# Kernel tuning notes

Hardware: AMD Instinct MI355X
Metric: run time of the kernel (lower is better)

Reference implementation:

```python
import jax, jax.numpy as jnp
import numpy as np

OUT = 3      # pooled output size (fmap_size//4 = 14//4 = 3)
RATIO = 2    # roi_align sampling ratio (fixed; torchvision adaptive ratio for 14/3 bins is 2)
P = 20       # num_persons


def _bilinear(fm, y, x):
    # fm: [C,H,W]; y,x broadcastable coordinate grids. torchvision aligned=False semantics.
    C, H, W = fm.shape
    y, x = jnp.broadcast_arrays(y, x)
    valid = (y > -1.0) & (y < H) & (x > -1.0) & (x < W)
    y = jnp.clip(y, 0.0, H - 1.0)
    x = jnp.clip(x, 0.0, W - 1.0)
    y0 = jnp.floor(y).astype(jnp.int32)
    x0 = jnp.floor(x).astype(jnp.int32)
    y1 = jnp.minimum(y0 + 1, H - 1)
    x1 = jnp.minimum(x0 + 1, W - 1)
    ly = y - y0
    lx = x - x0
    hy = 1.0 - ly
    hx = 1.0 - lx
    v00 = fm[:, y0, x0]
    v01 = fm[:, y0, x1]
    v10 = fm[:, y1, x0]
    v11 = fm[:, y1, x1]
    val = hy * hx * v00 + hy * lx * v01 + ly * hx * v10 + ly * lx * v11
    return jnp.where(valid, val, 0.0)  # [C, ...]


def _roi_align_one(fm, box):
    # fm: [C,H,W], box: [4] = (x1,y1,x2,y2) in feature-map coords -> [C,OUT,OUT]
    x1, y1, x2, y2 = box
    bw = (x2 - x1) / OUT
    bh = (y2 - y1) / OUT
    off = (jnp.arange(OUT * RATIO, dtype=fm.dtype) + 0.5) / RATIO  # bin-unit offsets
    xs = x1 + off * bw
    ys = y1 + off * bh
    vals = _bilinear(fm, ys[:, None], xs[None, :])  # [C, OUT*RATIO, OUT*RATIO]
    C = fm.shape[0]
    return vals.reshape(C, OUT, RATIO, OUT, RATIO).mean(axis=(2, 4))


def setup_inputs() -> dict:
    key = jax.random.key(0)
    ks = jax.random.split(key, 8)
    B, N, NB, C, FS = 128, 8, 27, 1024, 14
    fmap = jax.random.normal(ks[0], (B, C, FS, FS), jnp.float32)
    # boxes in feature-map coordinates with x1<x2, y1<y2
    lo = jax.random.uniform(ks[1], (B, N, 2), jnp.float32) * 10.0
    ext = 2.0 + jax.random.uniform(ks[2], (B, N, 2), jnp.float32) * 4.0
    hi = jnp.minimum(lo + ext, float(FS))
    boxes = jnp.concatenate([lo, hi], axis=-1)  # [B,N,4] (x1,y1,x2,y2)
    # unique person ids per frame (scatter target indices)
    pids = jax.vmap(lambda k: jax.random.permutation(k, P)[:N])(jax.random.split(ks[3], B)).astype(jnp.int32)
    w1 = jax.random.normal(ks[4], (512, C), jnp.float32) * 0.02
    w2 = jax.random.normal(ks[5], (256, 512), jnp.float32) * 0.05
    fc1_w = jax.random.normal(ks[6], (1024, 256 * OUT * OUT), jnp.float32) * 0.02
    fc1_b = jnp.zeros((1024,), jnp.float32)
    fc2_w = jax.random.normal(ks[7], (27, 1024), jnp.float32) * 0.02
    fc2_b = jnp.zeros((27,), jnp.float32)
    return {"fmap": fmap, "boxes": boxes, "pids": pids, "w1": w1, "w2": w2,
            "fc1_w": fc1_w, "fc1_b": fc1_b, "fc2_w": fc2_w, "fc2_b": fc2_b}


def _forward(fmap, boxes, pids, w1, w2, fc1_w, fc1_b, fc2_w, fc2_b):
    B, N = boxes.shape[:2]
    # per-image, per-box ROI align: [B,N,C,3,3]
    roi = jax.vmap(jax.vmap(_roi_align_one, in_axes=(None, 0)), in_axes=(0, 0))(fmap, boxes)
    # behavior_conv: two bias-free 1x1 convs (no nonlinearity between)
    h = jnp.einsum('bnchw,oc->bnohw', roi, w1)
    h = jnp.einsum('bnchw,oc->bnohw', h, w2)  # [B,N,256,3,3]
    feat = h.reshape(B, N, -1)                # [B,N,2304]
    bidx = jnp.broadcast_to(jnp.arange(B)[:, None], (B, N))
    # scatter into behavior_tensor keyed by person id (unique pids per frame -> well-defined)
    bt = jnp.zeros((B, P, feat.shape[-1]), feat.dtype).at[bidx, pids].set(feat)
    mean_b = bt.mean(axis=0)                  # [P,2304] mean over batch
    cur = bt[bidx, pids]                      # [B,N,2304]
    diff = mean_b[pids] - cur
    # behavior_fc (dropout is identity at inference)
    h1 = jax.nn.relu(jnp.einsum('bnd,hd->bnh', diff, fc1_w) + fc1_b)
    return jnp.einsum('bnh,oh->bno', h1, fc2_w) + fc2_b  # [B,N,num_behaviors]


def reference(fmap, boxes, pids, w1, w2, fc1_w, fc1_b, fc2_w, fc2_b):
    # fmap is detached and roi_align runs under no_grad in the original
    return _forward(jax.lax.stop_gradient(fmap), jax.lax.stop_gradient(boxes), pids,
                    w1, w2, fc1_w, fc1_b, fc2_w, fc2_b)
```

## Files before the change

kernel.cpp:

```cpp
#include <hip/hip_runtime.h>
#include <hip/hip_bf16.h>
#include <cstddef>
#include <cstdint>

#define B_   128
#define N_   8
#define C_   1024
#define FS_  14
#define POS_ 196
#define P_   20
#define HWC_ 9
#define CMID_ 256
#define FEATD_ 2304
#define H1_  1024
#define O_   27
#define PROWS_ (B_*N_*HWC_)

typedef __attribute__((ext_vector_type(8))) short bf16x8;
typedef __attribute__((ext_vector_type(4))) float f32x4;

__device__ __forceinline__ void gld16(const void* g, void* l) {
    __builtin_amdgcn_global_load_lds(
        (const __attribute__((address_space(1))) unsigned int*)g,
        (__attribute__((address_space(3))) unsigned int*)l, 16, 0, 0);
}

__global__ __launch_bounds__(256) void wcombine_split_kernel(
    const float* __restrict__ w1,
    const float* __restrict__ w2,
    float* __restrict__ wpart)
{
    const int tid = threadIdx.x;
    const int tx = tid & 15, ty = tid >> 4;
    const int c0 = blockIdx.x * 64;
    const int o0 = blockIdx.y * 64;
    const int kb = blockIdx.z * 64;
    __shared__ __align__(16) float As[16][68];
    __shared__ __align__(16) float Bs[16][68];
    float acc[4][4] = {};
    for (int k0 = kb; k0 < kb + 64; k0 += 16) {
        for (int i = tid; i < 64 * 16; i += 256) {
            int k = i & 15, m = i >> 4;
            As[k][m] = w2[(size_t)(o0 + m) * 512 + k0 + k];
        }
        for (int i = tid; i < 64 * 16; i += 256) {
            int n = i & 63, k = i >> 6;
            Bs[k][n] = w1[(size_t)(k0 + k) * 1024 + c0 + n];
        }
        __syncthreads();
        #pragma unroll
        for (int k = 0; k < 16; ++k) {
            float4 a = *(const float4*)&As[k][ty * 4];
            float4 b = *(const float4*)&Bs[k][tx * 4];
            float av[4] = {a.x, a.y, a.z, a.w};
            float bv[4] = {b.x, b.y, b.z, b.w};
            #pragma unroll
            for (int i = 0; i < 4; ++i)
                #pragma unroll
                for (int j = 0; j < 4; ++j)
                    acc[i][j] += av[i] * bv[j];
        }
        __syncthreads();
    }
    float* dst = wpart + (size_t)blockIdx.z * (256 * 1024);
    for (int i = 0; i < 4; ++i) {
        float4 v = make_float4(acc[i][0], acc[i][1], acc[i][2], acc[i][3]);
        *(float4*)&dst[(size_t)(o0 + ty * 4 + i) * 1024 + c0 + tx * 4] = v;
    }
}

__global__ __launch_bounds__(256) void wc_reduce_kernel(
    const float* __restrict__ wpart, __hip_bfloat16* __restrict__ Wc)
{
    int idx = blockIdx.x * 256 + threadIdx.x;
    float s = 0.f;
    #pragma unroll
    for (int z = 0; z < 8; ++z) s += wpart[(size_t)z * (256 * 1024) + idx];
    Wc[idx] = __float2bfloat16(s);
}

#define CCH_   64
#define SSTR_  232
#define AROWS_ 72
#define AOFF_  (AROWS_ * SSTR_)
struct bf4s { __hip_bfloat162 lo, hi; };
__global__ __launch_bounds__(256, 2) void roipool_kernel(
    const float* __restrict__ fmap,
    const float* __restrict__ boxes,
    __hip_bfloat16* __restrict__ pooled)
{
    const int b  = blockIdx.y;
    const int c0 = blockIdx.x * CCH_;
    const int tid = threadIdx.x;
    __shared__ __align__(16) __hip_bfloat16 Ls[(AROWS_ + CCH_) * SSTR_];

    float4 vbuf[13];
    const float* src = fmap + ((size_t)b * C_ + c0) * POS_;
    #pragma unroll
    for (int it = 0; it < 13; ++it) {
        int i = tid + it * 256;
        if (i < CCH_ * 49) {
            int c = i / 49, ch = i - c * 49;
            vbuf[it] = *(const float4*)(src + (size_t)c * POS_ + ch * 4);
        }
    }

    if (tid < AROWS_) {
        const int m = tid;
        const int n = m / 9, cell = m - n * 9;
        const int chh = cell / 3, cww = cell % 3;
        float4 bx = *(const float4*)(boxes + ((size_t)b * N_ + n) * 4);
        float bw = (bx.z - bx.x) * (1.0f / 3.0f);
        float bh = (bx.w - bx.y) * (1.0f / 3.0f);
        float ypro[FS_], xpro[FS_];
        #pragma unroll
        for (int k = 0; k < FS_; ++k) { ypro[k] = 0.f; xpro[k] = 0.f; }
        #pragma unroll
        for (int s = 0; s < 2; ++s) {
            float yy = bx.y + ((float)(2 * chh + s) + 0.5f) * 0.5f * bh;
            bool vy = (yy > -1.0f) && (yy < (float)FS_);
            float y = fminf(fmaxf(yy, 0.0f), (float)(FS_ - 1));
            int y0 = (int)floorf(y);
            int y1i = min(y0 + 1, FS_ - 1);
            float ly = y - (float)y0, hy = 1.0f - ly;
            float qy = vy ? 0.5f : 0.0f;
            float w0 = hy * qy, w1 = ly * qy;
            #pragma unroll
            for (int k = 0; k < FS_; ++k)
                ypro[k] += (k == y0 ? w0 : 0.f) + (k == y1i ? w1 : 0.f);
            float xx = bx.x + ((float)(2 * cww + s) + 0.5f) * 0.5f * bw;
            bool vx = (xx > -1.0f) && (xx < (float)FS_);
            float x = fminf(fmaxf(xx, 0.0f), (float)(FS_ - 1));
            int x0 = (int)floorf(x);
            int x1i = min(x0 + 1, FS_ - 1);
            float lx = x - (float)x0, hx = 1.0f - lx;
            float qx = vx ? 0.5f : 0.0f;
            float u0 = hx * qx, u1 = lx * qx;
            #pragma unroll
            for (int k = 0; k < FS_; ++k)
                xpro[k] += (k == x0 ? u0 : 0.f) + (k == x1i ? u1 : 0.f);
        }
        __hip_bfloat162* row2 = (__hip_bfloat162*)&Ls[m * SSTR_];
        #pragma unroll
        for (int p = 0; p < 98; ++p) {
            const int i0 = 2 * p, i1 = 2 * p + 1;
            __hip_bfloat162 t;
            t.x = __float2bfloat16(ypro[i0 / FS_] * xpro[i0 % FS_]);
            t.y = __float2bfloat16(ypro[i1 / FS_] * xpro[i1 % FS_]);
            row2[p] = t;
        }
        const __hip_bfloat16 z16 = __float2bfloat16(0.0f);
        #pragma unroll
        for (int p = 98; p < SSTR_ / 2; ++p) {
            __hip_bfloat162 t; t.x = z16; t.y = z16;
            row2[p] = t;
        }
    }

    #pragma unroll
    for (int it = 0; it < 13; ++it) {
        int i = tid + it * 256;
        if (i < CCH_ * 49) {
            int c = i / 49, ch = i - c * 49;
            float4 v = vbuf[it];
            bf4s t;
            t.lo.x = __float2bfloat16(v.x); t.lo.y = __float2bfloat16(v.y);
            t.hi.x = __float2bfloat16(v.z); t.hi.y = __float2bfloat16(v.w);
            *(bf4s*)&Ls[AOFF_ + c * SSTR_ + ch * 4] = t;
        }
    }
    {
        #pragma unroll
        for (int it = 0; it < 5; ++it) {
            int i = tid + it * 256;
            if (i < CCH_ * 18) {
                int r = i / 18, kd = i - r * 18;
                *(unsigned int*)&Ls[AOFF_ + r * SSTR_ + 196 + kd * 2] = 0;
            }
        }
    }
    __syncthreads();

    const int wave = tid >> 6, lane = tid & 63;
    const int m16 = lane & 15, quad = lane >> 4;
    f32x4 acc[5];
    #pragma unroll
    for (int mt = 0; mt < 5; ++mt) acc[mt] = (f32x4){0.f, 0.f, 0.f, 0.f};

    const int nrow = wave * 16 + m16;
    #pragma unroll
    for (int kk = 0; kk < 7; ++kk) {
        bf16x8 bfv = *(const bf16x8*)&Ls[AOFF_ + nrow * SSTR_ + kk * 32 + quad * 8];
        #pragma unroll
        for (int mt = 0; mt < 5; ++mt) {
            bf16x8 af = *(const bf16x8*)&Ls[(mt * 16 + m16) * SSTR_ + kk * 32 + quad * 8];
            acc[mt] = __builtin_amdgcn_mfma_f32_16x16x32_bf16(af, bfv, acc[mt], 0, 0, 0);
        }
    }

    const int col = c0 + wave * 16 + m16;
    #pragma unroll
    for (int mt = 0; mt < 5; ++mt) {
        #pragma unroll
        for (int g = 0; g < 4; ++g) {
            int row = mt * 16 + quad * 4 + g;
            if (row < AROWS_)
                pooled[(size_t)(b * AROWS_ + row) * C_ + col] =
                    __float2bfloat16(acc[mt][g]);
        }
    }
}

__global__ __launch_bounds__(256, 4) void pooledgemm_kernel(
    const __hip_bfloat16* __restrict__ A,
    const __hip_bfloat16* __restrict__ Bm,
    float* __restrict__ Cout)
{
    const int tid = threadIdx.x;
    const int wave = tid >> 6, lane = tid & 63;
    const int r0 = blockIdx.y * 64, n0 = blockIdx.x * 64;
    const int wm = (wave >> 1) * 32, wn = (wave & 1) * 32;
    const int m16 = lane & 15, quad = lane >> 4;
    const int K = C_;
    __shared__ __align__(16) __hip_bfloat16 As[64 * 64];
    __shared__ __align__(16) __hip_bfloat16 Bs[64 * 64];

    f32x4 acc[2][2];
    #pragma unroll
    for (int i = 0; i < 2; ++i)
        #pragma unroll
        for (int j = 0; j < 2; ++j)
            acc[i][j] = (f32x4){0.f, 0.f, 0.f, 0.f};

    const int qa = wave * 64 + lane;
    const int ms0 = qa >> 3, cs0 = (qa & 7) ^ (ms0 & 7);
    const int qb1 = qa + 256;
    const int ms1 = qb1 >> 3, cs1 = (qb1 & 7) ^ (ms1 & 7);
    const size_t rA0 = (size_t)(r0 + ms0) * K + cs0 * 8;
    const size_t rA1 = (size_t)(r0 + ms1) * K + cs1 * 8;
    const size_t rB0 = (size_t)(n0 + ms0) * K + cs0 * 8;
    const size_t rB1 = (size_t)(n0 + ms1) * K + cs1 * 8;

    for (int k0 = 0; k0 < K; k0 += 64) {
        gld16(A  + rA0 + k0, &As[wave * 512]);
        gld16(Bm + rB0 + k0, &Bs[wave * 512]);
        gld16(A  + rA1 + k0, &As[2048 + wave * 512]);
        gld16(Bm + rB1 + k0, &Bs[2048 + wave * 512]);
        __syncthreads();
        #pragma unroll
        for (int ks = 0; ks < 2; ++ks) {
            bf16x8 af[2], bfv[2];
            #pragma unroll
            for (int t = 0; t < 2; ++t) {
                int m = wm + t * 16 + m16;
                int cp = (ks * 4 + quad) ^ (m & 7);
                af[t] = *(const bf16x8*)&As[(m * 8 + cp) * 8];
                int n = wn + t * 16 + m16;
                int cq = (ks * 4 + quad) ^ (n & 7);
                bfv[t] = *(const bf16x8*)&Bs[(n * 8 + cq) * 8];
            }
            #pragma unroll
            for (int i = 0; i < 2; ++i)
                #pragma unroll
                for (int j = 0; j < 2; ++j)
                    acc[i][j] = __builtin_amdgcn_mfma_f32_16x16x32_bf16(
                        af[i], bfv[j], acc[i][j], 0, 0, 0);
        }
        __syncthreads();
    }

    #pragma unroll
    for (int i = 0; i < 2; ++i) {
        #pragma unroll
        for (int j = 0; j < 2; ++j) {
            int col = n0 + wn + j * 16 + m16;
            int rbase = r0 + wm + i * 16 + quad * 4;
            #pragma unroll
            for (int g = 0; g < 4; ++g)
                Cout[(size_t)(rbase + g) * 256 + col] = acc[i][j][g];
        }
    }
}

__global__ __launch_bounds__(256, 4) void fc1_gemm_kernel(
    const __hip_bfloat16* __restrict__ A,
    const __hip_bfloat16* __restrict__ Bm,
    const float* __restrict__ bias,
    float* __restrict__ C)
{
    const int tid = threadIdx.x;
    const int wave = tid >> 6, lane = tid & 63;
    const int r0 = blockIdx.y * 32, n0 = blockIdx.x * 64;
    const int wm = (wave >> 1) * 16, wn = (wave & 1) * 32;
    const int m16 = lane & 15, quad = lane >> 4;
    const int K = FEATD_;
    __shared__ __align__(16) __hip_bfloat16 As[32 * 64];
    __shared__ __align__(16) __hip_bfloat16 Bs[64 * 64];

    f32x4 acc[2];
    acc[0] = (f32x4){0.f, 0.f, 0.f, 0.f};
    acc[1] = (f32x4){0.f, 0.f, 0.f, 0.f};

    const int qa = wave * 64 + lane;
    const int msA = qa >> 3, csA = (qa & 7) ^ (msA & 7);
    const int qb1 = qa + 256;
    const int msB1 = qb1 >> 3, csB1 = (qb1 & 7) ^ (msB1 & 7);
    const size_t rA  = (size_t)(r0 + msA)  * K + csA  * 8;
    const size_t rB0 = (size_t)(n0 + msA)  * K + csA  * 8;
    const size_t rB1 = (size_t)(n0 + msB1) * K + csB1 * 8;

    for (int k0 = 0; k0 < K; k0 += 64) {
        gld16(A  + rA  + k0, &As[wave * 512]);
        gld16(Bm + rB0 + k0, &Bs[wave * 512]);
        gld16(Bm + rB1 + k0, &Bs[2048 + wave * 512]);
        __syncthreads();
        #pragma unroll
        for (int ks = 0; ks < 2; ++ks) {
            bf16x8 af, bfv[2];
            int m = wm + m16;
            int cp = (ks * 4 + quad) ^ (m & 7);
            af = *(const bf16x8*)&As[(m * 8 + cp) * 8];
            #pragma unroll
            for (int t = 0; t < 2; ++t) {
                int n = wn + t * 16 + m16;
                int cq = (ks * 4 + quad) ^ (n & 7);
                bfv[t] = *(const bf16x8*)&Bs[(n * 8 + cq) * 8];
            }
            #pragma unroll
            for (int j = 0; j < 2; ++j)
                acc[j] = __builtin_amdgcn_mfma_f32_16x16x32_bf16(
                    af, bfv[j], acc[j], 0, 0, 0);
        }
        __syncthreads();
    }

    #pragma unroll
    for (int j = 0; j < 2; ++j) {
        int col = n0 + wn + j * 16 + m16;
        int rbase = r0 + wm + quad * 4;
        float bv = bias[col];
        #pragma unroll
        for (int g = 0; g < 4; ++g) {
            int r = rbase + g;
            float v = acc[j][g] + bv;
            C[(size_t)r * H1_ + col] = v > 0.f ? v : 0.f;
        }
    }
}

__global__ __launch_bounds__(256) void fc1w_perm_kernel(
    const float* __restrict__ src, __hip_bfloat16* __restrict__ dst)
{
    int h = blockIdx.x;
    int tid = threadIdx.x;
    __shared__ float buf[FEATD_];
    const float* s = src + (size_t)h * FEATD_;
    #pragma unroll
    for (int it = 0; it < 9; ++it)
        buf[it * 256 + tid] = s[it * 256 + tid];
    __syncthreads();
    __hip_bfloat16* d = dst + (size_t)h * FEATD_;
    #pragma unroll
    for (int it = 0; it < 9; ++it) {
        int dd = it * 256 + tid;
        d[dd] = __float2bfloat16(buf[tid * HWC_ + it]);
    }
}

__global__ __launch_bounds__(64) void invmap_kernel(
    const int* __restrict__ pids, int* __restrict__ inv)
{
    int b = blockIdx.x;
    int p = threadIdx.x;
    if (p < P_) {
        int v = -1;
        for (int n = 0; n < N_; ++n)
            if (pids[b * N_ + n] == p) v = n;
        inv[b * P_ + p] = v;
    }
}

__global__ __launch_bounds__(256) void meandiff_kernel(
    const float* __restrict__ feat, const int* __restrict__ inv,
    __hip_bfloat16* __restrict__ diff)
{
    int p = blockIdx.x;
    int d = blockIdx.y * 256 + threadIdx.x;
    float acc = 0.0f;
    #pragma unroll 4
    for (int b = 0; b < B_; ++b) {
        int n = inv[b * P_ + p];
        if (n >= 0) acc += feat[(size_t)(b * N_ + n) * FEATD_ + d];
    }
    float mean = acc * (1.0f / (float)B_);
    #pragma unroll 4
    for (int b = 0; b < B_; ++b) {
        int n = inv[b * P_ + p];
        if (n >= 0) {
            size_t r = (size_t)(b * N_ + n);
            diff[r * FEATD_ + d] = __float2bfloat16(mean - feat[r * FEATD_ + d]);
        }
    }
}

__global__ __launch_bounds__(256) void fc2_kernel(
    const float* __restrict__ h1, const float* __restrict__ fc2_w,
    const float* __restrict__ fc2_b, float* __restrict__ out)
{
    int bn = blockIdx.x;
    int tid = threadIdx.x;
    __shared__ __align__(16) float row[H1_];
    __shared__ float partial[32][8];
    ((float4*)row)[tid] = ((const float4*)(h1 + (size_t)bn * H1_))[tid];
    __syncthreads();
    int o = tid >> 3, part = tid & 7;
    float acc = 0.0f;
    if (o < O_) {
        const float* wrow = fc2_w + (size_t)o * H1_ + part * 128;
        const float* hrow = row + part * 128;
        #pragma unroll 4
        for (int j = 0; j < 128; ++j) acc += hrow[j] * wrow[j];
    }
    partial[o][part] = acc;
    __syncthreads();
    if (part == 0 && o < O_) {
        float s = fc2_b[o];
        #pragma unroll
        for (int p = 0; p < 8; ++p) s += partial[o][p];
        out[(size_t)bn * O_ + o] = s;
    }
}

extern "C" void kernel_launch(void* const* d_in, const int* in_sizes, int n_in,
                              void* d_out, int out_size, void* d_ws, size_t ws_size,
                              hipStream_t stream) {
    const float* fmap  = (const float*)d_in[0];
    const float* boxes = (const float*)d_in[1];
    const int*   pids  = (const int*)  d_in[2];
    const float* w1    = (const float*)d_in[3];
    const float* w2    = (const float*)d_in[4];
    const float* fc1_w = (const float*)d_in[5];
    const float* fc1_b = (const float*)d_in[6];
    const float* fc2_w = (const float*)d_in[7];
    const float* fc2_b = (const float*)d_in[8];
    float* out = (float*)d_out;

    char* wsb = (char*)d_ws;
    __hip_bfloat16* Wc     = (__hip_bfloat16*)wsb;
    __hip_bfloat16* pooled = Wc + 256 * 1024;
    __hip_bfloat16* fc1wp  = pooled + (size_t)PROWS_ * C_;
    __hip_bfloat16* diffp  = fc1wp + (size_t)H1_ * FEATD_;
    float* feat   = (float*)(diffp + (size_t)H1_ * FEATD_);
    float* mean_b = feat + (size_t)(B_ * N_) * FEATD_;
    float* h1     = mean_b + (size_t)P_ * FEATD_;
    int*   inv    = (int*)(h1 + (size_t)(B_ * N_) * H1_);
    float* wpart  = (float*)(inv + 128 * P_ + 64);

    hipLaunchKernelGGL(wcombine_split_kernel, dim3(16, 4, 8), dim3(256), 0, stream,
                       w1, w2, wpart);
    hipLaunchKernelGGL(wc_reduce_kernel, dim3(1024), dim3(256), 0, stream,
                       wpart, Wc);
    hipLaunchKernelGGL(roipool_kernel, dim3(C_ / CCH_, 128), dim3(256), 0, stream,
                       fmap, boxes, pooled);
    hipLaunchKernelGGL(pooledgemm_kernel, dim3(4, 144), dim3(256), 0, stream,
                       pooled, Wc, feat);
    hipLaunchKernelGGL(fc1w_perm_kernel, dim3(1024), dim3(256), 0, stream,
                       fc1_w, fc1wp);
    hipLaunchKernelGGL(invmap_kernel, dim3(128), dim3(64), 0, stream,
                       pids, inv);
    hipLaunchKernelGGL(meandiff_kernel, dim3(20, 9), dim3(256), 0, stream,
                       feat, inv, diffp);
    hipLaunchKernelGGL(fc1_gemm_kernel, dim3(16, 32), dim3(256), 0, stream,
                       diffp, fc1wp, fc1_b, h1);
    hipLaunchKernelGGL(fc2_kernel, dim3(1024), dim3(256), 0, stream,
                       h1, fc2_w, fc2_b, out);
}
```

Baseline: 303.4 us.

## Fuse ROI pooling with channel-mixing GEMM and fold inverse map into meandiff

Merges the ROI-align pooling kernel and the pooled×Wc GEMM into one kernel. Each block pools 64-channel chunks into shared memory and immediately multiplies them by the combined weight, accumulating over 512 channels. Two channel halves write separate partial outputs that meandiff sums, so the bf16 pooled intermediate never round-trips through global memory. The inverse person map is now built inside meandiff, which removes a launch. The grid shrinks to 256 blocks with serialized chunk loops, so the risk is lower parallelism and less latency hiding, plus extra partial-sum traffic.

```diff
diff --git a/kernel.cpp b/kernel.cpp
--- a/kernel.cpp
+++ b/kernel.cpp
@@ -14,7 +14,6 @@
 #define FEATD_ 2304
 #define H1_  1024
 #define O_   27
-#define PROWS_ (B_*N_*HWC_)
 
 typedef __attribute__((ext_vector_type(8))) short bf16x8;
 typedef __attribute__((ext_vector_type(4))) float f32x4;
@@ -79,31 +78,24 @@
     Wc[idx] = __float2bfloat16(s);
 }
 
-#define CCH_   64
 #define SSTR_  232
 #define AROWS_ 72
-#define AOFF_  (AROWS_ * SSTR_)
+#define BOFF_  (AROWS_ * SSTR_)
+#define PSTR_  72
+#define POFF_  (BOFF_ + 64 * SSTR_)
 struct bf4s { __hip_bfloat162 lo, hi; };
-__global__ __launch_bounds__(256, 2) void roipool_kernel(
+__global__ __launch_bounds__(256, 2) void poolmix_kernel(
     const float* __restrict__ fmap,
     const float* __restrict__ boxes,
-    __hip_bfloat16* __restrict__ pooled)
-{
+    const __hip_bfloat16* __restrict__ Wc,
+    float* __restrict__ featp)
+{
+    const int cq = blockIdx.x;
     const int b  = blockIdx.y;
-    const int c0 = blockIdx.x * CCH_;
     const int tid = threadIdx.x;
-    __shared__ __align__(16) __hip_bfloat16 Ls[(AROWS_ + CCH_) * SSTR_];
-
-    float4 vbuf[13];
-    const float* src = fmap + ((size_t)b * C_ + c0) * POS_;
-    #pragma unroll
-    for (int it = 0; it < 13; ++it) {
-        int i = tid + it * 256;
-        if (i < CCH_ * 49) {
-            int c = i / 49, ch = i - c * 49;
-            vbuf[it] = *(const float4*)(src + (size_t)c * POS_ + ch * 4);
-        }
-    }
+    const int wave = tid >> 6, lane = tid & 63;
+    const int m16 = lane & 15, quad = lane >> 4;
+    __shared__ __align__(16) __hip_bfloat16 Ls[POFF_ + AROWS_ * PSTR_];
 
     if (tid < AROWS_) {
         const int m = tid;
@@ -156,128 +148,90 @@
             row2[p] = t;
         }
     }
-
-    #pragma unroll
-    for (int it = 0; it < 13; ++it) {
-        int i = tid + it * 256;
-        if (i < CCH_ * 49) {
-            int c = i / 49, ch = i - c * 49;
-            float4 v = vbuf[it];
-            bf4s t;
-            t.lo.x = __float2bfloat16(v.x); t.lo.y = __float2bfloat16(v.y);
-            t.hi.x = __float2bfloat16(v.z); t.hi.y = __float2bfloat16(v.w);
-            *(bf4s*)&Ls[AOFF_ + c * SSTR_ + ch * 4] = t;
-        }
-    }
-    {
-        #pragma unroll
-        for (int it = 0; it < 5; ++it) {
+    for (int i = tid; i < 64 * 18; i += 256) {
+        int r = i / 18, kd = i - r * 18;
+        *(unsigned int*)&Ls[BOFF_ + r * SSTR_ + 196 + kd * 2] = 0;
+    }
+
+    f32x4 acc2[5][4];
+    #pragma unroll
+    for (int mt = 0; mt < 5; ++mt)
+        #pragma unroll
+        for (int nt = 0; nt < 4; ++nt)
+            acc2[mt][nt] = (f32x4){0.f, 0.f, 0.f, 0.f};
+
+    const int cbase0 = cq * 512;
+    for (int c = 0; c < 8; ++c) {
+        const float* src = fmap + ((size_t)b * C_ + cbase0 + c * 64) * POS_;
+        #pragma unroll
+        for (int it = 0; it < 13; ++it) {
             int i = tid + it * 256;
-            if (i < CCH_ * 18) {
-                int r = i / 18, kd = i - r * 18;
-                *(unsigned int*)&Ls[AOFF_ + r * SSTR_ + 196 + kd * 2] = 0;
-            }
-        }
-    }
-    __syncthreads();
-
-    const int wave = tid >> 6, lane = tid & 63;
-    const int m16 = lane & 15, quad = lane >> 4;
-    f32x4 acc[5];
-    #pragma unroll
-    for (int mt = 0; mt < 5; ++mt) acc[mt] = (f32x4){0.f, 0.f, 0.f, 0.f};
-
-    const int nrow = wave * 16 + m16;
-    #pragma unroll
-    for (int kk = 0; kk < 7; ++kk) {
-        bf16x8 bfv = *(const bf16x8*)&Ls[AOFF_ + nrow * SSTR_ + kk * 32 + quad * 8];
+            if (i < 64 * 49) {
+                int cr = i / 49, ch = i - cr * 49;
+                float4 v = *(const float4*)(src + (size_t)cr * POS_ + ch * 4);
+                bf4s t;
+                t.lo.x = __float2bfloat16(v.x); t.lo.y = __float2bfloat16(v.y);
+                t.hi.x = __float2bfloat16(v.z); t.hi.y = __float2bfloat16(v.w);
+                *(bf4s*)&Ls[BOFF_ + cr * SSTR_ + ch * 4] = t;
+            }
+        }
+        __syncthreads();
+
+        f32x4 acc1[5];
+        #pragma unroll
+        for (int mt = 0; mt < 5; ++mt) acc1[mt] = (f32x4){0.f, 0.f, 0.f, 0.f};
+        const int nrow = wave * 16 + m16;
+        #pragma unroll
+        for (int kk = 0; kk < 7; ++kk) {
+            bf16x8 bfv = *(const bf16x8*)&Ls[BOFF_ + nrow * SSTR_ + kk * 32 + quad * 8];
+            #pragma unroll
+            for (int mt = 0; mt < 5; ++mt) {
+                bf16x8 af = *(const bf16x8*)&Ls[(mt * 16 + m16) * SSTR_ + kk * 32 + quad * 8];
+                acc1[mt] = __builtin_amdgcn_mfma_f32_16x16x32_bf16(af, bfv, acc1[mt], 0, 0, 0);
+            }
+        }
         #pragma unroll
         for (int mt = 0; mt < 5; ++mt) {
-            bf16x8 af = *(const bf16x8*)&Ls[(mt * 16 + m16) * SSTR_ + kk * 32 + quad * 8];
-            acc[mt] = __builtin_amdgcn_mfma_f32_16x16x32_bf16(af, bfv, acc[mt], 0, 0, 0);
-        }
-    }
-
-    const int col = c0 + wave * 16 + m16;
+            #pragma unroll
+            for (int g = 0; g < 4; ++g) {
+                int cell = mt * 16 + quad * 4 + g;
+                if (cell < AROWS_)
+                    Ls[POFF_ + cell * PSTR_ + wave * 16 + m16] =
+                        __float2bfloat16(acc1[mt][g]);
+            }
+        }
+        __syncthreads();
+
+        #pragma unroll
+        for (int ks = 0; ks < 2; ++ks) {
+            bf16x8 af[5];
+            #pragma unroll
+            for (int mt = 0; mt < 5; ++mt)
+                af[mt] = *(const bf16x8*)&Ls[POFF_ + (mt * 16 + m16) * PSTR_ + ks * 32 + quad * 8];
+            #pragma unroll
+            for (int nt = 0; nt < 4; ++nt) {
+                int n = wave * 64 + nt * 16 + m16;
+                bf16x8 bfv = *(const bf16x8*)(Wc + (size_t)n * C_ + cbase0 + c * 64 + ks * 32 + quad * 8);
+                #pragma unroll
+                for (int mt = 0; mt < 5; ++mt)
+                    acc2[mt][nt] = __builtin_amdgcn_mfma_f32_16x16x32_bf16(
+                        af[mt], bfv, acc2[mt][nt], 0, 0, 0);
+            }
+        }
+    }
+
+    float* dst = featp + (size_t)cq * (128 * AROWS_ * 256);
     #pragma unroll
     for (int mt = 0; mt < 5; ++mt) {
         #pragma unroll
         for (int g = 0; g < 4; ++g) {
             int row = mt * 16 + quad * 4 + g;
-            if (row < AROWS_)
-                pooled[(size_t)(b * AROWS_ + row) * C_ + col] =
-                    __float2bfloat16(acc[mt][g]);
-        }
-    }
-}
-
-__global__ __launch_bounds__(256, 4) void pooledgemm_kernel(
-    const __hip_bfloat16* __restrict__ A,
-    const __hip_bfloat16* __restrict__ Bm,
-    float* __restrict__ Cout)
-{
-    const int tid = threadIdx.x;
-    const int wave = tid >> 6, lane = tid & 63;
-    const int r0 = blockIdx.y * 64, n0 = blockIdx.x * 64;
-    const int wm = (wave >> 1) * 32, wn = (wave & 1) * 32;
-    const int m16 = lane & 15, quad = lane >> 4;
-    const int K = C_;
-    __shared__ __align__(16) __hip_bfloat16 As[64 * 64];
-    __shared__ __align__(16) __hip_bfloat16 Bs[64 * 64];
-
-    f32x4 acc[2][2];
-    #pragma unroll
-    for (int i = 0; i < 2; ++i)
-        #pragma unroll
-        for (int j = 0; j < 2; ++j)
-            acc[i][j] = (f32x4){0.f, 0.f, 0.f, 0.f};
-
-    const int qa = wave * 64 + lane;
-    const int ms0 = qa >> 3, cs0 = (qa & 7) ^ (ms0 & 7);
-    const int qb1 = qa + 256;
-    const int ms1 = qb1 >> 3, cs1 = (qb1 & 7) ^ (ms1 & 7);
-    const size_t rA0 = (size_t)(r0 + ms0) * K + cs0 * 8;
-    const size_t rA1 = (size_t)(r0 + ms1) * K + cs1 * 8;
-    const size_t rB0 = (size_t)(n0 + ms0) * K + cs0 * 8;
-    const size_t rB1 = (size_t)(n0 + ms1) * K + cs1 * 8;
-
-    for (int k0 = 0; k0 < K; k0 += 64) {
-        gld16(A  + rA0 + k0, &As[wave * 512]);
-        gld16(Bm + rB0 + k0, &Bs[wave * 512]);
-        gld16(A  + rA1 + k0, &As[2048 + wave * 512]);
-        gld16(Bm + rB1 + k0, &Bs[2048 + wave * 512]);
-        __syncthreads();
-        #pragma unroll
-        for (int ks = 0; ks < 2; ++ks) {
-            bf16x8 af[2], bfv[2];
-            #pragma unroll
-            for (int t = 0; t < 2; ++t) {
-                int m = wm + t * 16 + m16;
-                int cp = (ks * 4 + quad) ^ (m & 7);
-                af[t] = *(const bf16x8*)&As[(m * 8 + cp) * 8];
-                int n = wn + t * 16 + m16;
-                int cq = (ks * 4 + quad) ^ (n & 7);
-                bfv[t] = *(const bf16x8*)&Bs[(n * 8 + cq) * 8];
-            }
-            #pragma unroll
-            for (int i = 0; i < 2; ++i)
+            if (row < AROWS_) {
                 #pragma unroll
-                for (int j = 0; j < 2; ++j)
-                    acc[i][j] = __builtin_amdgcn_mfma_f32_16x16x32_bf16(
-                        af[i], bfv[j], acc[i][j], 0, 0, 0);
-        }
-        __syncthreads();
-    }
-
-    #pragma unroll
-    for (int i = 0; i < 2; ++i) {
-        #pragma unroll
-        for (int j = 0; j < 2; ++j) {
-            int col = n0 + wn + j * 16 + m16;
-            int rbase = r0 + wm + i * 16 + quad * 4;
-            #pragma unroll
-            for (int g = 0; g < 4; ++g)
-                Cout[(size_t)(rbase + g) * 256 + col] = acc[i][j][g];
+                for (int nt = 0; nt < 4; ++nt)
+                    dst[(size_t)(b * AROWS_ + row) * 256 + wave * 64 + nt * 16 + m16] =
+                        acc2[mt][nt][g];
+            }
         }
     }
 }
@@ -367,38 +321,39 @@
     }
 }
 
-__global__ __launch_bounds__(64) void invmap_kernel(
-    const int* __restrict__ pids, int* __restrict__ inv)
-{
-    int b = blockIdx.x;
-    int p = threadIdx.x;
-    if (p < P_) {
-        int v = -1;
-        for (int n = 0; n < N_; ++n)
-            if (pids[b * N_ + n] == p) v = n;
-        inv[b * P_ + p] = v;
-    }
-}
-
 __global__ __launch_bounds__(256) void meandiff_kernel(
-    const float* __restrict__ feat, const int* __restrict__ inv,
-    __hip_bfloat16* __restrict__ diff)
+    const float* __restrict__ fp0, const float* __restrict__ fp1,
+    const int* __restrict__ pids, __hip_bfloat16* __restrict__ diff)
 {
     int p = blockIdx.x;
     int d = blockIdx.y * 256 + threadIdx.x;
+    __shared__ int invs[B_];
+    if (threadIdx.x < B_) {
+        int bb = threadIdx.x;
+        int v = -1;
+        #pragma unroll
+        for (int n = 0; n < N_; ++n)
+            if (pids[bb * N_ + n] == p) v = n;
+        invs[bb] = v;
+    }
+    __syncthreads();
+
     float acc = 0.0f;
     #pragma unroll 4
     for (int b = 0; b < B_; ++b) {
-        int n = inv[b * P_ + p];
-        if (n >= 0) acc += feat[(size_t)(b * N_ + n) * FEATD_ + d];
+        int n = invs[b];
+        if (n >= 0) {
+            size_t idx = (size_t)(b * N_ + n) * FEATD_ + d;
+            acc += fp0[idx] + fp1[idx];
+        }
     }
     float mean = acc * (1.0f / (float)B_);
     #pragma unroll 4
     for (int b = 0; b < B_; ++b) {
-        int n = inv[b * P_ + p];
+        int n = invs[b];
         if (n >= 0) {
-            size_t r = (size_t)(b * N_ + n);
-            diff[r * FEATD_ + d] = __float2bfloat16(mean - feat[r * FEATD_ + d]);
+            size_t idx = (size_t)(b * N_ + n) * FEATD_ + d;
+            diff[idx] = __float2bfloat16(mean - (fp0[idx] + fp1[idx]));
         }
     }
 }
@@ -446,30 +401,25 @@
     float* out = (float*)d_out;
 
     char* wsb = (char*)d_ws;
-    __hip_bfloat16* Wc     = (__hip_bfloat16*)wsb;
-    __hip_bfloat16* pooled = Wc + 256 * 1024;
-    __hip_bfloat16* fc1wp  = pooled + (size_t)PROWS_ * C_;
-    __hip_bfloat16* diffp  = fc1wp + (size_t)H1_ * FEATD_;
-    float* feat   = (float*)(diffp + (size_t)H1_ * FEATD_);
-    float* mean_b = feat + (size_t)(B_ * N_) * FEATD_;
-    float* h1     = mean_b + (size_t)P_ * FEATD_;
-    int*   inv    = (int*)(h1 + (size_t)(B_ * N_) * H1_);
-    float* wpart  = (float*)(inv + 128 * P_ + 64);
+    __hip_bfloat16* Wc    = (__hip_bfloat16*)wsb;
+    __hip_bfloat16* fc1wp = Wc + 256 * 1024;
+    __hip_bfloat16* diffp = fc1wp + (size_t)H1_ * FEATD_;
+    float* featp  = (float*)(diffp + (size_t)H1_ * FEATD_);
+    float* h1     = featp + 2 * (size_t)(B_ * N_) * FEATD_;
+    float* wpart  = h1 + (size_t)(B_ * N_) * H1_;
+    float* fp0 = featp;
+    float* fp1 = featp + (size_t)(B_ * N_) * FEATD_;
 
     hipLaunchKernelGGL(wcombine_split_kernel, dim3(16, 4, 8), dim3(256), 0, stream,
                        w1, w2, wpart);
     hipLaunchKernelGGL(wc_reduce_kernel, dim3(1024), dim3(256), 0, stream,
                        wpart, Wc);
-    hipLaunchKernelGGL(roipool_kernel, dim3(C_ / CCH_, 128), dim3(256), 0, stream,
-                       fmap, boxes, pooled);
-    hipLaunchKernelGGL(pooledgemm_kernel, dim3(4, 144), dim3(256), 0, stream,
-                       pooled, Wc, feat);
+    hipLaunchKernelGGL(poolmix_kernel, dim3(2, 128), dim3(256), 0, stream,
+                       fmap, boxes, Wc, featp);
     hipLaunchKernelGGL(fc1w_perm_kernel, dim3(1024), dim3(256), 0, stream,
                        fc1_w, fc1wp);
-    hipLaunchKernelGGL(invmap_kernel, dim3(128), dim3(64), 0, stream,
-                       pids, inv);
     hipLaunchKernelGGL(meandiff_kernel, dim3(20, 9), dim3(256), 0, stream,
-                       feat, inv, diffp);
+                       fp0, fp1, pids, diffp);
     hipLaunchKernelGGL(fc1_gemm_kernel, dim3(16, 32), dim3(256), 0, stream,
                        diffp, fc1wp, fc1_b, h1);
     hipLaunchKernelGGL(fc2_kernel, dim3(1024), dim3(256), 0, stream,
```

Result: no change. 297.9 us (-1.8%).
